# Kernel optimization log

Hardware: AMD Instinct MI355X
Metric: run time of the kernel (lower is better)

## Reference

```python
import math
import jax, jax.numpy as jnp
import numpy as np

D = 768      # hidden_size
H = 16       # num_attention_heads (hardcoded in module)
DH = D // H  # value dim per head
SEQ = 512    # fpos/tpos are taken modulo 512
EPS = 1e-5   # torch LayerNorm default
SCALE = math.sqrt(D / H)  # attention_head_size = dim_key_query_all / num_heads


def _collab_attn(h, fpos, tpos, Wq, Wk, Wcb, Wv, bv, mix, Wd, bd, lng, lnb):
    """CollaborativeAttention.forward on one segment. h: [SEQ, D]."""
    fpos = fpos % SEQ
    tpos = tpos % SEQ
    fs = h[fpos]                                   # [F, D] gathered 'from' nodes
    ts = h[tpos]                                   # [T, D] gathered 'to' nodes
    q = fs @ Wq.T                                  # [F, D] (no bias)
    k = ts @ Wk.T                                  # [T, D] (no bias)
    mq = q[None, :, :] * mix[:, None, :]           # [H, F, D] per-head mixing
    scores = jnp.einsum('hfd,td->hft', mq, k)      # [H, F, T] full-D contraction
    cb = (ts @ Wcb.T).T                            # [H, T] content bias
    scores = (scores + cb[:, None, :]) / SCALE
    probs = jax.nn.softmax(scores, axis=-1)        # dropout = identity at eval
    v = (ts @ Wv.T + bv).reshape(-1, H, DH).transpose(1, 0, 2)  # [H, T, DH]
    ctx = jnp.einsum('hft,htd->hfd', probs, v)     # [H, F, DH]
    ctx = ctx.transpose(1, 0, 2).reshape(-1, D) @ Wd.T + bd      # [F, D]
    x = fs + ctx                                   # residual on gathered nodes
    mu = x.mean(-1, keepdims=True)
    var = ((x - mu) ** 2).mean(-1, keepdims=True)
    return lng * (x - mu) / jnp.sqrt(var + EPS) + lnb


def _encoder(hidden_states, fpos, tpos, qtoc, ctoq):
    outs = []
    for b in range(3):  # fixed small segment count, matches original unrolling
        o1 = _collab_attn(hidden_states[b], fpos[b], tpos[b], *qtoc).mean(0)
        o2 = _collab_attn(hidden_states[b], tpos[b], fpos[b], *ctoq).mean(0)
        outs.append(jnp.concatenate([o1, o2]))
    return jnp.stack(outs)  # [3, 2*D]


def setup_inputs() -> dict:
    key = jax.random.key(0)
    ks = jax.random.split(key, 32)
    inp = {
        'hidden_states': jax.random.normal(ks[0], (3, SEQ, D), jnp.float32),
        'fpos': jax.random.randint(ks[1], (3, 2048), 0, SEQ, jnp.int32),
        'tpos': jax.random.randint(ks[2], (3, 2048), 0, SEQ, jnp.int32),
    }
    i = 3
    for p in ('qtoc', 'ctoq'):
        for n, shape, std in (('Wq', (D, D), 0.02), ('Wk', (D, D), 0.02),
                              ('Wcb', (H, D), 0.02), ('Wv', (D, D), 0.02),
                              ('Wd', (D, D), 0.02), ('mix', (H, D), 0.2)):
            inp[p + '_' + n] = std * jax.random.normal(ks[i], shape, jnp.float32)
            i += 1
        inp[p + '_bv'] = jnp.zeros((D,), jnp.float32)
        inp[p + '_bd'] = jnp.zeros((D,), jnp.float32)
        inp[p + '_lng'] = jnp.ones((D,), jnp.float32)
        inp[p + '_lnb'] = jnp.zeros((D,), jnp.float32)
    return inp


def reference(hidden_states, fpos, tpos,
              qtoc_Wq, qtoc_Wk, qtoc_Wcb, qtoc_Wv, qtoc_Wd, qtoc_mix,
              qtoc_bv, qtoc_bd, qtoc_lng, qtoc_lnb,
              ctoq_Wq, ctoq_Wk, ctoq_Wcb, ctoq_Wv, ctoq_Wd, ctoq_mix,
              ctoq_bv, ctoq_bd, ctoq_lng, ctoq_lnb):
    qtoc = (qtoc_Wq, qtoc_Wk, qtoc_Wcb, qtoc_Wv, qtoc_bv, qtoc_mix,
            qtoc_Wd, qtoc_bd, qtoc_lng, qtoc_lnb)
    ctoq = (ctoq_Wq, ctoq_Wk, ctoq_Wcb, ctoq_Wv, ctoq_bv, ctoq_mix,
            ctoq_Wd, ctoq_bd, ctoq_lng, ctoq_lnb)
    return _encoder(hidden_states, fpos, tpos, qtoc, ctoq)
```

## Files before the change

### kernel.cpp

```cpp
#include <hip/hip_runtime.h>
#include <math.h>

#define DD 768
#define HH 16
#define DHH 48
#define NPOS 512
#define NIDX 2048
#define INV_SCALE 0.14433756729740643f
#define LN_EPS 1e-5f

typedef __bf16 bf16_t;
typedef __bf16 bf16x8 __attribute__((ext_vector_type(8)));
typedef float f32x4 __attribute__((ext_vector_type(4)));

__device__ __forceinline__ void g2lds16(const void* g, void* l) {
  __builtin_amdgcn_global_load_lds((const __attribute__((address_space(1))) void*)g,
                                   (__attribute__((address_space(3))) void*)l, 16, 0, 0);
}
__device__ __forceinline__ int stg_chunk(int lane) { return (lane & 3) ^ ((lane >> 3) & 3); }
__device__ __forceinline__ int rd_off(int row, int lq) {
  return row * 32 + ((lq ^ ((row >> 1) & 3)) << 3);
}

struct CvtDesc { const float* src; bf16_t* dst; int n8; };
struct CvtBatch { CvtDesc d[13]; };

__global__ __launch_bounds__(256) void prep(const int* __restrict__ fpos,
                                            const int* __restrict__ tpos,
                                            int* __restrict__ CNT, CvtBatch cvb) {
  const int bid = blockIdx.x;
  const int tid = threadIdx.x;
  __shared__ int shist[NPOS];
  if (bid < 6) {
    const int b = bid >> 1, which = bid & 1;
    const int* src = (which ? tpos : fpos) + b * NIDX;
    for (int i = tid; i < NPOS; i += 256) shist[i] = 0;
    __syncthreads();
    for (int i = tid; i < NIDX; i += 256) atomicAdd(&shist[src[i] & (NPOS - 1)], 1);
    __syncthreads();
    for (int i = tid; i < NPOS; i += 256) CNT[bid * NPOS + i] = shist[i];
    return;
  }
  const CvtDesc de = cvb.d[(bid - 6) >> 6];
  for (int i = ((bid - 6) & 63) * 256 + tid; i < de.n8; i += 64 * 256) {
    bf16_t t[8];
    if (de.src) {
      const f32x4 a = *(const f32x4*)(de.src + (size_t)i * 8);
      const f32x4 b = *(const f32x4*)(de.src + (size_t)i * 8 + 4);
#pragma unroll
      for (int e = 0; e < 4; ++e) { t[e] = (bf16_t)a[e]; t[4 + e] = (bf16_t)b[e]; }
    } else {
#pragma unroll
      for (int e = 0; e < 8; ++e) t[e] = (bf16_t)0.f;
    }
    *(bf16x8*)(de.dst + (size_t)i * 8) = *(bf16x8*)t;
  }
}

struct MDesc { const bf16_t* A; const bf16_t* B; const float* bias; void* C;
               float* cb; int mode; int ntiles; };
struct MBatch { MDesc d[18]; };

__global__ __launch_bounds__(256, 4) void gemm64(MBatch batch) {
  const MDesc de = batch.d[blockIdx.y];
  const int mt = blockIdx.x & 7, nt = blockIdx.x >> 3;
  if (nt >= de.ntiles) return;
  const int m0 = mt * 64, n0 = nt * 128;

  __shared__ bf16_t SA[2][2048];
  __shared__ bf16_t SB[2][4096];

  const int tid = threadIdx.x;
  const int w = tid >> 6, lane = tid & 63;
  const int wm = w >> 1, wn = w & 1;
  const int lm = lane & 15, lq = lane >> 4;
  const int sr = lane >> 2, sc = stg_chunk(lane);

  f32x4 acc[2][4] = {};

  auto stage = [&](int buf, int k0) {
#pragma unroll
    for (int c = 0; c < 3; ++c) {
      const int issue = w + c * 4;
      if (issue < 4)
        g2lds16(de.A + (size_t)(m0 + issue * 16 + sr) * 768 + k0 + sc * 8,
                SA[buf] + issue * 512);
      else {
        const int e = issue - 4;
        g2lds16(de.B + (size_t)(n0 + e * 16 + sr) * 768 + k0 + sc * 8,
                SB[buf] + e * 512);
      }
    }
  };

  stage(0, 0);
  for (int k0i = 0; k0i < 24; ++k0i) {
    const int cur = k0i & 1;
    __syncthreads();
    if (k0i + 1 < 24) stage(cur ^ 1, (k0i + 1) * 32);
    bf16x8 af[2], bfr[4];
#pragma unroll
    for (int i = 0; i < 2; ++i)
      af[i] = *(const bf16x8*)(SA[cur] + rd_off(wm * 32 + i * 16 + lm, lq));
#pragma unroll
    for (int j = 0; j < 4; ++j)
      bfr[j] = *(const bf16x8*)(SB[cur] + rd_off(wn * 64 + j * 16 + lm, lq));
#pragma unroll
    for (int i = 0; i < 2; ++i)
#pragma unroll
      for (int j = 0; j < 4; ++j)
        acc[i][j] = __builtin_amdgcn_mfma_f32_16x16x32_bf16(af[i], bfr[j], acc[i][j], 0, 0, 0);
  }

#pragma unroll
  for (int i = 0; i < 2; ++i) {
    const int rbase = m0 + wm * 32 + i * 16 + lq * 4;
#pragma unroll
    for (int j = 0; j < 4; ++j) {
      const int c = n0 + wn * 64 + j * 16 + lm;
      const float bv = (de.bias && c < 768) ? de.bias[c] : 0.f;
#pragma unroll
      for (int r = 0; r < 4; ++r) {
        const float v = acc[i][j][r] + bv;
        if (de.mode == 0)      ((float*)de.C)[(size_t)(rbase + r) * 768 + c] = v;
        else if (de.mode == 1) ((bf16_t*)de.C)[(size_t)(rbase + r) * 768 + c] = (bf16_t)v;
        else if (de.mode == 2) ((bf16_t*)de.C)[(size_t)c * NPOS + rbase + r] = (bf16_t)v;
        else {
          if (c < 768)       ((bf16_t*)de.C)[(size_t)(rbase + r) * 768 + c] = (bf16_t)v;
          else if (c < 784)  de.cb[(size_t)(rbase + r) * 16 + (c - 768)] = v;
        }
      }
    }
  }
}

__global__ __launch_bounds__(256, 2) void attn_mfma(
    const bf16_t* __restrict__ Qg, const bf16_t* __restrict__ Kg,
    const bf16_t* __restrict__ Vt, const float* __restrict__ cbG,
    const int* __restrict__ CNT, const float* __restrict__ mix0,
    const float* __restrict__ mix1, bf16_t* __restrict__ CTX) {
  const int bid = blockIdx.x;
  const int ft = bid & 7, h = (bid >> 3) & 15, pd = bid >> 7;
  const int dir = pd & 1;
  const int f0 = ft * 64;

  __shared__ bf16_t U[36864];
  __shared__ float mixs[768];
  __shared__ float cbw[512];
  __shared__ float rowl[64];

  const int tid = threadIdx.x;
  const int w = tid >> 6, lane = tid & 63;
  const bf16_t* Qp = Qg + (size_t)pd * NPOS * DD;
  const bf16_t* Kp = Kg + (size_t)pd * NPOS * DD;
  const bf16_t* Vp = Vt + (size_t)pd * DD * NPOS + (size_t)h * DHH * NPOS;
  const float* mix = (dir ? mix1 : mix0) + h * DD;
  const int* cnt = CNT + ((pd & ~1) + (1 - dir)) * NPOS;

  for (int i = tid; i < 768; i += 256) mixs[i] = mix[i] * INV_SCALE;
  for (int i = tid; i < 512; i += 256)
    cbw[i] = cbG[((size_t)pd * NPOS + i) * HH + h] * INV_SCALE + __logf((float)cnt[i]);

  const int lm = lane & 15, lq = lane >> 4;
  const int sr = lane >> 2, sc = stg_chunk(lane);

  int qoff[4], koff[8];
#pragma unroll
  for (int i = 0; i < 4; ++i) qoff[i] = rd_off(i * 16 + lm, lq);
#pragma unroll
  for (int j = 0; j < 8; ++j) koff[j] = 2048 + w * 4096 + rd_off(j * 16 + lm, lq);

  auto stage = [&](int buf, int k0) {
    bf16_t* base = U + buf * 18432;
    g2lds16(Qp + (size_t)(f0 + w * 16 + sr) * DD + k0 + sc * 8, base + w * 512);
#pragma unroll
    for (int e = 0; e < 8; ++e)
      g2lds16(Kp + (size_t)(w * 128 + e * 16 + sr) * DD + k0 + sc * 8,
              base + 2048 + w * 4096 + e * 512);
  };

  f32x4 sa[32];
#pragma unroll
  for (int t = 0; t < 32; ++t) sa[t] = (f32x4){0.f, 0.f, 0.f, 0.f};

  stage(0, 0);
  for (int k0i = 0; k0i < 24; ++k0i) {
    const int cur = k0i & 1;
    __syncthreads();
    if (k0i + 1 < 24) stage(cur ^ 1, (k0i + 1) * 32);
    const bf16_t* base = U + cur * 18432;
    const int k0 = k0i * 32;
    const f32x4 mxa = *(const f32x4*)&mixs[k0 + lq * 8];
    const f32x4 mxb = *(const f32x4*)&mixs[k0 + lq * 8 + 4];
    bf16x8 af[4];
#pragma unroll
    for (int i = 0; i < 4; ++i) {
      const bf16x8 q = *(const bf16x8*)(base + qoff[i]);
      bf16_t t[8];
#pragma unroll
      for (int e = 0; e < 4; ++e) {
        t[e]     = (bf16_t)((float)q[e] * mxa[e]);
        t[4 + e] = (bf16_t)((float)q[4 + e] * mxb[e]);
      }
      af[i] = *(bf16x8*)t;
    }
#pragma unroll
    for (int j = 0; j < 8; ++j) {
      const bf16x8 bf = *(const bf16x8*)(base + koff[j]);
#pragma unroll
      for (int i = 0; i < 4; ++i)
        sa[i * 8 + j] = __builtin_amdgcn_mfma_f32_16x16x32_bf16(af[i], bf, sa[i * 8 + j], 0, 0, 0);
    }
  }

  f32x4 pv[4] = {};
  for (int jt = 0; jt < 4; ++jt) {
    const int j0 = jt * 128;
    __syncthreads();

    for (int i = tid; i < 49 * 16; i += 256) {
      const int r = i >> 4, cc = i & 15;
      if (r < 48)
        *(bf16x8*)(U + 8704 + r * 136 + cc * 8) =
            *(const bf16x8*)(Vp + (size_t)r * NPOS + j0 + cc * 8);
      else {
        bf16_t ones[8];
#pragma unroll
        for (int e = 0; e < 8; ++e) ones[e] = (bf16_t)1.f;
        *(bf16x8*)(U + 8704 + 48 * 136 + cc * 8) = *(bf16x8*)ones;
      }
    }
    if (w == jt) {
#pragma unroll
      for (int jj = 0; jj < 8; ++jj) {
        const int col = jj * 16 + lm;
        const float cb = cbw[j0 + col];
#pragma unroll
        for (int i = 0; i < 4; ++i) {
          const int rb = i * 16 + lq * 4;
#pragma unroll
          for (int r = 0; r < 4; ++r)
            U[(rb + r) * 136 + col] = (bf16_t)__expf(sa[i * 8 + jj][r] + cb);
        }
      }
    }
    __syncthreads();

#pragma unroll
    for (int kk = 0; kk < 4; ++kk) {
      const bf16x8 pa = *(const bf16x8*)(U + (w * 16 + lm) * 136 + kk * 32 + lq * 8);
#pragma unroll
      for (int j = 0; j < 4; ++j) {
        const bf16x8 pb = *(const bf16x8*)(U + 8704 + (j * 16 + lm) * 136 + kk * 32 + lq * 8);
        pv[j] = __builtin_amdgcn_mfma_f32_16x16x32_bf16(pa, pb, pv[j], 0, 0, 0);
      }
    }
  }

  if (lm == 0) {
#pragma unroll
    for (int r = 0; r < 4; ++r) rowl[w * 16 + lq * 4 + r] = pv[3][r];
  }
  __syncthreads();
#pragma unroll
  for (int j = 0; j < 3; ++j) {
#pragma unroll
    for (int r = 0; r < 4; ++r) {
      const int fr = w * 16 + lq * 4 + r;
      CTX[((size_t)pd * NPOS + f0 + fr) * DD + h * DHH + j * 16 + lm] =
          (bf16_t)(pv[j][r] / rowl[fr]);
    }
  }
}

__global__ __launch_bounds__(256) void ln_mean_kernel(
    const float* __restrict__ hs, const float* __restrict__ XB,
    const int* __restrict__ CNT,
    const float* __restrict__ lng0, const float* __restrict__ lnb0,
    const float* __restrict__ lng1, const float* __restrict__ lnb1,
    float* __restrict__ out) {
  const int blk = blockIdx.x;
  const int chunk = blk & 63;
  const int pd = blk >> 6;
  const int b = pd >> 1, dir = pd & 1;
  const float* lng = dir ? lng1 : lng0;
  const float* lnb = dir ? lnb1 : lnb0;
  const int* cnt = CNT + pd * NPOS;
  const float* hb = hs + (size_t)b * NPOS * DD;
  const float* xb = XB + (size_t)pd * NPOS * DD;

  __shared__ float wacc[4][DD];
  const int tid = threadIdx.x;
  const int wave = tid >> 6, lane = tid & 63;
  for (int d0 = tid; d0 < 4 * DD; d0 += 256) ((float*)wacc)[d0] = 0.f;
  __syncthreads();

  float lg[12], lb[12];
#pragma unroll
  for (int qd = 0; qd < 12; ++qd) {
    lg[qd] = lng[lane + qd * 64];
    lb[qd] = lnb[lane + qd * 64];
  }

  for (int rr = 0; rr < 2; ++rr) {
    const int p = chunk * 8 + wave * 2 + rr;
    float x[12];
    float s = 0.f, ss = 0.f;
#pragma unroll
    for (int qd = 0; qd < 12; ++qd) {
      const int d0 = lane + qd * 64;
      const float xv = hb[(size_t)p * DD + d0] + xb[(size_t)p * DD + d0];
      x[qd] = xv; s += xv; ss += xv * xv;
    }
#pragma unroll
    for (int o = 1; o < 64; o <<= 1) {
      s += __shfl_xor(s, o);
      ss += __shfl_xor(ss, o);
    }
    const float mu = s * (1.f / 768.f);
    const float var = ss * (1.f / 768.f) - mu * mu;
    const float rstd = rsqrtf(var + LN_EPS);
    const float wgt = (float)cnt[p];
    if (wgt != 0.f) {
#pragma unroll
      for (int qd = 0; qd < 12; ++qd) {
        const int d0 = lane + qd * 64;
        wacc[wave][d0] += wgt * (lg[qd] * (x[qd] - mu) * rstd + lb[qd]);
      }
    }
  }
  __syncthreads();
  for (int d0 = tid; d0 < DD; d0 += 256) {
    const float t = wacc[0][d0] + wacc[1][d0] + wacc[2][d0] + wacc[3][d0];
    atomicAdd(&out[b * 1536 + dir * 768 + d0], t * (1.f / 2048.f));
  }
}

extern "C" void kernel_launch(void* const* d_in, const int* in_sizes, int n_in,
                              void* d_out, int out_size, void* d_ws, size_t ws_size,
                              hipStream_t stream) {
  const float* hs  = (const float*)d_in[0];
  const int* fpos  = (const int*)d_in[1];
  const int* tpos  = (const int*)d_in[2];

  const float* Wq[2]; const float* Wk[2]; const float* Wcb[2]; const float* Wv[2];
  const float* Wd[2]; const float* mixp[2];
  const float* bv[2]; const float* bd[2]; const float* lng[2]; const float* lnb[2];
  for (int p = 0; p < 2; ++p) {
    const int base = 3 + p * 10;
    Wq[p]   = (const float*)d_in[base + 0];
    Wk[p]   = (const float*)d_in[base + 1];
    Wcb[p]  = (const float*)d_in[base + 2];
    Wv[p]   = (const float*)d_in[base + 3];
    Wd[p]   = (const float*)d_in[base + 4];
    mixp[p] = (const float*)d_in[base + 5];
    bv[p]   = (const float*)d_in[base + 6];
    bd[p]   = (const float*)d_in[base + 7];
    lng[p]  = (const float*)d_in[base + 8];
    lnb[p]  = (const float*)d_in[base + 9];
  }

  char* wsp = (char*)d_ws;
  size_t off = 0;
  auto alloc = [&](size_t bytes) { char* p = wsp + off; off = (off + bytes + 255) & ~(size_t)255; return p; };
  bf16_t* hsb  = (bf16_t*)alloc((size_t)3 * NPOS * DD * 2);
  bf16_t* Wb   = (bf16_t*)alloc((size_t)6 * DD * DD * 2);
  bf16_t* WkCb = (bf16_t*)alloc((size_t)2 * 896 * DD * 2);
  bf16_t* Qbf  = (bf16_t*)alloc((size_t)6 * NPOS * DD * 2);
  bf16_t* Kbf  = (bf16_t*)alloc((size_t)6 * NPOS * DD * 2);
  bf16_t* VtG  = (bf16_t*)alloc((size_t)6 * DD * NPOS * 2);
  bf16_t* CTXb = (bf16_t*)alloc((size_t)6 * NPOS * DD * 2);
  float*  XB   = (float*) alloc((size_t)6 * NPOS * DD * 4);
  float*  cbG  = (float*) alloc((size_t)6 * NPOS * HH * 4);
  int*    CNTb = (int*)   alloc((size_t)6 * NPOS * 4);

  hipMemsetAsync(d_out, 0, (size_t)out_size * sizeof(float), stream);

  CvtBatch cvb{};
  cvb.d[0] = CvtDesc{hs, hsb, 3 * NPOS * DD / 8};
  for (int p = 0; p < 2; ++p) {
    cvb.d[1 + p * 3] = CvtDesc{Wq[p], Wb + (size_t)(p * 3 + 0) * DD * DD, DD * DD / 8};
    cvb.d[2 + p * 3] = CvtDesc{Wv[p], Wb + (size_t)(p * 3 + 1) * DD * DD, DD * DD / 8};
    cvb.d[3 + p * 3] = CvtDesc{Wd[p], Wb + (size_t)(p * 3 + 2) * DD * DD, DD * DD / 8};
    bf16_t* wk = WkCb + (size_t)p * 896 * DD;
    cvb.d[7 + p * 3] = CvtDesc{Wk[p], wk, DD * DD / 8};
    cvb.d[8 + p * 3] = CvtDesc{Wcb[p], wk + (size_t)768 * DD, 16 * DD / 8};
    cvb.d[9 + p * 3] = CvtDesc{nullptr, wk + (size_t)784 * DD, 112 * DD / 8};
  }
  prep<<<838, 256, 0, stream>>>(fpos, tpos, CNTb, cvb);

  MBatch gb{};
  int n = 0;
  for (int b = 0; b < 3; ++b)
    for (int p = 0; p < 2; ++p) {
      const int pd = b * 2 + p;
      const bf16_t* A = hsb + (size_t)b * NPOS * DD;
      const size_t o = (size_t)pd * NPOS * DD;
      gb.d[n++] = MDesc{A, Wb + (size_t)(p * 3 + 0) * DD * DD, nullptr, Qbf + o, nullptr, 1, 6};
      gb.d[n++] = MDesc{A, WkCb + (size_t)p * 896 * DD, nullptr, Kbf + o,
                        cbG + (size_t)pd * NPOS * HH, 3, 7};
      gb.d[n++] = MDesc{A, Wb + (size_t)(p * 3 + 1) * DD * DD, bv[p],
                        VtG + (size_t)pd * DD * NPOS, nullptr, 2, 6};
    }
  gemm64<<<dim3(56, 18), 256, 0, stream>>>(gb);

  attn_mfma<<<768, 256, 0, stream>>>(Qbf, Kbf, VtG, cbG, CNTb, mixp[0], mixp[1], CTXb);

  MBatch gd{};
  for (int b = 0; b < 3; ++b)
    for (int p = 0; p < 2; ++p) {
      const int pd = b * 2 + p;
      const size_t o = (size_t)pd * NPOS * DD;
      gd.d[pd] = MDesc{CTXb + o, Wb + (size_t)(p * 3 + 2) * DD * DD, bd[p],
                       XB + o, nullptr, 0, 6};
    }
  gemm64<<<dim3(56, 6), 256, 0, stream>>>(gd);

  ln_mean_kernel<<<384, 256, 0, stream>>>(hs, XB, CNTb, lng[0], lnb[0], lng[1], lnb[1],
                                          (float*)d_out);
}
```

Before: 263.6 us.

## Restructure attention kernel to compute scores per key tile, cutting registers and LDS

The attention kernel no longer computes the full 64x512 score tile up front in 128 accumulator registers per thread. It now recomputes QK scores for each 128-column key tile inside the jt loop, with a 2x2 warp split, and the exp/store work is spread across all warps instead of one. This shrinks LDS (smaller U buffer, bf16 mix) and register pressure so launch bounds can allow 4 blocks per CU. The cost is that Q tiles are restaged for each key tile, there are more barriers, and mixing is now done in bf16 (q*mix multiplied in bf16), which slightly changes precision.

Measured after the change: 245.8 us. 6.8% less time.

```diff
diff --git a/kernel.cpp b/kernel.cpp
--- a/kernel.cpp
+++ b/kernel.cpp
@@ -134,7 +134,7 @@
   }
 }
 
-__global__ __launch_bounds__(256, 2) void attn_mfma(
+__global__ __launch_bounds__(256, 4) void attn_mfma(
     const bf16_t* __restrict__ Qg, const bf16_t* __restrict__ Kg,
     const bf16_t* __restrict__ Vt, const float* __restrict__ cbG,
     const int* __restrict__ CNT, const float* __restrict__ mix0,
@@ -144,8 +144,8 @@
   const int dir = pd & 1;
   const int f0 = ft * 64;
 
-  __shared__ bf16_t U[36864];
-  __shared__ float mixs[768];
+  __shared__ bf16_t U[17408];
+  __shared__ bf16_t mixs[768];
   __shared__ float cbw[512];
   __shared__ float rowl[64];
 
@@ -157,67 +157,74 @@
   const float* mix = (dir ? mix1 : mix0) + h * DD;
   const int* cnt = CNT + ((pd & ~1) + (1 - dir)) * NPOS;
 
-  for (int i = tid; i < 768; i += 256) mixs[i] = mix[i] * INV_SCALE;
+  for (int i = tid; i < 768; i += 256) mixs[i] = (bf16_t)(mix[i] * INV_SCALE);
   for (int i = tid; i < 512; i += 256)
     cbw[i] = cbG[((size_t)pd * NPOS + i) * HH + h] * INV_SCALE + __logf((float)cnt[i]);
 
+  const int wm = w >> 1, wn = w & 1;
   const int lm = lane & 15, lq = lane >> 4;
   const int sr = lane >> 2, sc = stg_chunk(lane);
 
-  int qoff[4], koff[8];
-#pragma unroll
-  for (int i = 0; i < 4; ++i) qoff[i] = rd_off(i * 16 + lm, lq);
-#pragma unroll
-  for (int j = 0; j < 8; ++j) koff[j] = 2048 + w * 4096 + rd_off(j * 16 + lm, lq);
-
-  auto stage = [&](int buf, int k0) {
-    bf16_t* base = U + buf * 18432;
-    g2lds16(Qp + (size_t)(f0 + w * 16 + sr) * DD + k0 + sc * 8, base + w * 512);
-#pragma unroll
-    for (int e = 0; e < 8; ++e)
-      g2lds16(Kp + (size_t)(w * 128 + e * 16 + sr) * DD + k0 + sc * 8,
-              base + 2048 + w * 4096 + e * 512);
-  };
-
-  f32x4 sa[32];
-#pragma unroll
-  for (int t = 0; t < 32; ++t) sa[t] = (f32x4){0.f, 0.f, 0.f, 0.f};
-
-  stage(0, 0);
-  for (int k0i = 0; k0i < 24; ++k0i) {
-    const int cur = k0i & 1;
-    __syncthreads();
-    if (k0i + 1 < 24) stage(cur ^ 1, (k0i + 1) * 32);
-    const bf16_t* base = U + cur * 18432;
-    const int k0 = k0i * 32;
-    const f32x4 mxa = *(const f32x4*)&mixs[k0 + lq * 8];
-    const f32x4 mxb = *(const f32x4*)&mixs[k0 + lq * 8 + 4];
-    bf16x8 af[4];
-#pragma unroll
-    for (int i = 0; i < 4; ++i) {
-      const bf16x8 q = *(const bf16x8*)(base + qoff[i]);
-      bf16_t t[8];
-#pragma unroll
-      for (int e = 0; e < 4; ++e) {
-        t[e]     = (bf16_t)((float)q[e] * mxa[e]);
-        t[4 + e] = (bf16_t)((float)q[4 + e] * mxb[e]);
-      }
-      af[i] = *(bf16x8*)t;
-    }
-#pragma unroll
-    for (int j = 0; j < 8; ++j) {
-      const bf16x8 bf = *(const bf16x8*)(base + koff[j]);
-#pragma unroll
-      for (int i = 0; i < 4; ++i)
-        sa[i * 8 + j] = __builtin_amdgcn_mfma_f32_16x16x32_bf16(af[i], bf, sa[i * 8 + j], 0, 0, 0);
-    }
-  }
-
   f32x4 pv[4] = {};
+
   for (int jt = 0; jt < 4; ++jt) {
     const int j0 = jt * 128;
     __syncthreads();
 
+    auto stage = [&](int buf, int k0) {
+#pragma unroll
+      for (int c = 0; c < 3; ++c) {
+        const int issue = w + c * 4;
+        if (issue < 4)
+          g2lds16(Qp + (size_t)(f0 + issue * 16 + sr) * DD + k0 + sc * 8,
+                  U + buf * 6144 + issue * 512);
+        else {
+          const int e = issue - 4;
+          g2lds16(Kp + (size_t)(j0 + e * 16 + sr) * DD + k0 + sc * 8,
+                  U + buf * 6144 + 2048 + e * 512);
+        }
+      }
+    };
+
+    stage(0, 0);
+    f32x4 sa[2][4] = {};
+    for (int k0i = 0; k0i < 24; ++k0i) {
+      const int cur = k0i & 1;
+      __syncthreads();
+      if (k0i + 1 < 24) stage(cur ^ 1, (k0i + 1) * 32);
+      const bf16x8 mx = *(const bf16x8*)&mixs[k0i * 32 + lq * 8];
+      bf16x8 af[2], bfr[4];
+#pragma unroll
+      for (int i = 0; i < 2; ++i) {
+        const bf16x8 q = *(const bf16x8*)(U + cur * 6144 + rd_off(wm * 32 + i * 16 + lm, lq));
+        bf16_t t[8];
+#pragma unroll
+        for (int e = 0; e < 8; ++e) t[e] = (bf16_t)(q[e] * mx[e]);
+        af[i] = *(bf16x8*)t;
+      }
+#pragma unroll
+      for (int j = 0; j < 4; ++j)
+        bfr[j] = *(const bf16x8*)(U + cur * 6144 + 2048 + rd_off(wn * 64 + j * 16 + lm, lq));
+#pragma unroll
+      for (int i = 0; i < 2; ++i)
+#pragma unroll
+        for (int j = 0; j < 4; ++j)
+          sa[i][j] = __builtin_amdgcn_mfma_f32_16x16x32_bf16(af[i], bfr[j], sa[i][j], 0, 0, 0);
+    }
+    __syncthreads();
+
+#pragma unroll
+    for (int j = 0; j < 4; ++j) {
+      const int col = wn * 64 + j * 16 + lm;
+      const float cb = cbw[j0 + col];
+#pragma unroll
+      for (int i = 0; i < 2; ++i) {
+        const int rbase = wm * 32 + i * 16 + lq * 4;
+#pragma unroll
+        for (int r = 0; r < 4; ++r)
+          U[(rbase + r) * 136 + col] = (bf16_t)__expf(sa[i][j][r] + cb);
+      }
+    }
     for (int i = tid; i < 49 * 16; i += 256) {
       const int r = i >> 4, cc = i & 15;
       if (r < 48)
@@ -228,20 +235,6 @@
 #pragma unroll
         for (int e = 0; e < 8; ++e) ones[e] = (bf16_t)1.f;
         *(bf16x8*)(U + 8704 + 48 * 136 + cc * 8) = *(bf16x8*)ones;
-      }
-    }
-    if (w == jt) {
-#pragma unroll
-      for (int jj = 0; jj < 8; ++jj) {
-        const int col = jj * 16 + lm;
-        const float cb = cbw[j0 + col];
-#pragma unroll
-        for (int i = 0; i < 4; ++i) {
-          const int rb = i * 16 + lq * 4;
-#pragma unroll
-          for (int r = 0; r < 4; ++r)
-            U[(rb + r) * 136 + col] = (bf16_t)__expf(sa[i * 8 + jj][r] + cb);
-        }
       }
     }
     __syncthreads();
```
